# Kernel optimization log

Hardware: AMD Instinct MI355X
Metric: run time of the kernel (lower is better)

The kernel has to match this reference:

```python
import jax, jax.numpy as jnp
import numpy as np

MAX_DEPTH = 7
DEPTH_SIZES = [4 ** d for d in range(1, MAX_DEPTH + 1)]  # nodes per depth
N_NODES = sum(DEPTH_SIZES)  # 21844
N_TIMES = 48
HIDDEN = 1024
ENC_DIM = 256
B, S = 128, 32


def setup_inputs() -> dict:
    key = jax.random.key(0)
    k = jax.random.split(key, 6)
    return {
        "prefix_embedding": jax.random.normal(k[0], (B, S, HIDDEN), dtype=jnp.float32),
        "emb_matrix": jax.random.normal(k[1], (N_NODES, ENC_DIM), dtype=jnp.float32) * 0.02,
        "W_key": jax.random.normal(k[2], (HIDDEN, ENC_DIM), dtype=jnp.float32) * (1.0 / np.sqrt(ENC_DIM)),
        "b_key": jax.random.normal(k[3], (HIDDEN,), dtype=jnp.float32) * 0.01,
        "W_time": jax.random.normal(k[4], (N_TIMES, HIDDEN), dtype=jnp.float32) * (1.0 / np.sqrt(HIDDEN)),
        "b_time": jax.random.normal(k[5], (N_TIMES,), dtype=jnp.float32) * 0.01,
    }


def reference(prefix_embedding, emb_matrix, W_key, b_key, W_time, b_time):
    # keys = embedding_to_key(make_embedding_matrix(...)): [N_NODES, HIDDEN]
    keys = emb_matrix @ W_key.T + b_key
    # bmm(prefix [B,S,H], keys^T): keys identical across batch -> shared einsum
    scores = jnp.einsum("bsh,nh->bsn", prefix_embedding, keys)  # [B,S,N_NODES]
    # multitask: per-depth gather of the contiguous node block + log_softmax
    locations = []
    off = 0
    for n in DEPTH_SIZES:
        locations.append(jax.nn.log_softmax(scores[..., off:off + n], axis=-1))
        off += n
    time = jax.nn.log_softmax(prefix_embedding @ W_time.T + b_time, axis=-1)  # [B,S,N_TIMES]
    return tuple(locations) + (time,)
```

## Files before the change

### kernel.cpp

```cpp
#include <hip/hip_runtime.h>

#define NNODES 21844
#define ENC 256
#define HID 1024
#define ROWS 4096
#define NTIMES 48

typedef __attribute__((ext_vector_type(8))) short bf16x8;
typedef __attribute__((ext_vector_type(4))) float f32x4;

__device__ const int g_off[8] = {0, 4, 20, 84, 340, 1364, 5460, 21844};
__device__ const int g_l2[7]  = {2, 4, 6, 8, 10, 12, 14};

__device__ inline unsigned short f2bf(float f) {
  unsigned int u = __float_as_uint(f);
  u += 0x7FFF + ((u >> 16) & 1);
  return (unsigned short)(u >> 16);
}

__device__ inline int depth_of(int c) {
  return (c >= 4) + (c >= 20) + (c >= 84) + (c >= 340) + (c >= 1364) + (c >= 5460);
}

__global__ __launch_bounds__(256) void prep(const float* __restrict__ prefix,
                                            const float* __restrict__ emb,
                                            const float* __restrict__ Wk,
                                            const float* __restrict__ Wt,
                                            unsigned short* __restrict__ Pb16,
                                            unsigned short* __restrict__ Eb,
                                            unsigned short* __restrict__ WkT,
                                            float* __restrict__ WtT) {
  int bid = blockIdx.x, tid = threadIdx.x;
  if (bid < 4096) {
    int i = bid * 256 + tid;
    float4 v = reinterpret_cast<const float4*>(prefix)[i];
    ushort4 o; o.x = f2bf(v.x); o.y = f2bf(v.y); o.z = f2bf(v.z); o.w = f2bf(v.w);
    reinterpret_cast<ushort4*>(Pb16)[i] = o;
  } else if (bid < 9557) {
    int i = (bid - 4096) * 256 + tid;
    float4 v = reinterpret_cast<const float4*>(emb)[i];
    ushort4 o; o.x = f2bf(v.x); o.y = f2bf(v.y); o.z = f2bf(v.z); o.w = f2bf(v.w);
    reinterpret_cast<ushort4*>(Eb)[i] = o;
  } else if (bid < 10581) {
    int i = (bid - 9557) * 256 + tid;
    int e = i >> 10, h = i & 1023;
    WkT[i] = f2bf(Wk[h * ENC + e]);
  } else {
    int i = (bid - 10581) * 256 + tid;
    int k = i / NTIMES, c = i % NTIMES;
    WtT[i] = Wt[c * HID + k];
  }
}

__global__ __launch_bounds__(256) void p2_mfma(const unsigned short* __restrict__ Ab,
                                               const unsigned short* __restrict__ Bb,
                                               unsigned short* __restrict__ P2) {
  int lane = threadIdx.x & 63, w = threadIdx.x >> 6;
  int lr = lane & 15, lg = lane >> 4;
  int m0 = blockIdx.y * 64 + w * 16;
  int nb = blockIdx.x * 64;
  f32x4 acc[4];
#pragma unroll
  for (int n = 0; n < 4; ++n) acc[n] = f32x4{0.f, 0.f, 0.f, 0.f};
  const unsigned short* Ap = Ab + (long)(m0 + lr) * HID + lg * 8;
  for (int kk = 0; kk < 32; ++kk) {
    bf16x8 a = *reinterpret_cast<const bf16x8*>(Ap + kk * 32);
#pragma unroll
    for (int n = 0; n < 4; ++n) {
      bf16x8 b = *reinterpret_cast<const bf16x8*>(Bb + (long)(nb + n * 16 + lr) * HID + kk * 32 + lg * 8);
      acc[n] = __builtin_amdgcn_mfma_f32_16x16x32_bf16(a, b, acc[n], 0, 0, 0);
    }
  }
#pragma unroll
  for (int n = 0; n < 4; ++n)
#pragma unroll
    for (int j = 0; j < 4; ++j)
      P2[(m0 + lg * 4 + j) * ENC + nb + n * 16 + lr] = f2bf(acc[n][j]);
}

#define GEMM_TILE_BODY                                                                     \
  __shared__ unsigned short As[128 * 64];                                                  \
  __shared__ unsigned short Bs[128 * 64];                                                  \
  int tid = threadIdx.x;                                                                   \
  int lane = tid & 63, w = tid >> 6;                                                       \
  int lr = lane & 15, lg = lane >> 4;                                                      \
  int wr = w >> 1, wc = w & 1;                                                             \
  int m0 = blockIdx.x * 128, n0 = blockIdx.y * 128;                                        \
  int rr = tid >> 3, c8 = tid & 7;                                                         \
  f32x4 acc[4][4];                                                                         \
  _Pragma("unroll") for (int m = 0; m < 4; ++m)                                            \
    _Pragma("unroll") for (int n = 0; n < 4; ++n) acc[m][n] = f32x4{0.f, 0.f, 0.f, 0.f};   \
  for (int kt = 0; kt < 4; ++kt) {                                                         \
    if (kt) __syncthreads();                                                               \
    _Pragma("unroll") for (int r = 0; r < 4; ++r) {                                        \
      const unsigned short* ga = P2 + (long)(m0 + r * 32 + rr) * ENC + kt * 64 + c8 * 8;   \
      __builtin_amdgcn_global_load_lds(                                                    \
          (const __attribute__((address_space(1))) unsigned int*)ga,                       \
          (__attribute__((address_space(3))) unsigned int*)(As + r * 2048 + w * 512),      \
          16, 0, 0);                                                                       \
      int er = n0 + r * 32 + rr;                                                           \
      if (er > NNODES - 1) er = NNODES - 1;                                                \
      const unsigned short* gb = E + (long)er * ENC + kt * 64 + c8 * 8;                    \
      __builtin_amdgcn_global_load_lds(                                                    \
          (const __attribute__((address_space(1))) unsigned int*)gb,                       \
          (__attribute__((address_space(3))) unsigned int*)(Bs + r * 2048 + w * 512),      \
          16, 0, 0);                                                                       \
    }                                                                                      \
    __syncthreads();                                                                       \
    _Pragma("unroll") for (int kk = 0; kk < 2; ++kk) {                                     \
      bf16x8 a[4], b[4];                                                                   \
      _Pragma("unroll") for (int m = 0; m < 4; ++m)                                        \
        a[m] = *reinterpret_cast<const bf16x8*>(As + (wr * 64 + m * 16 + lr) * 64 + kk * 32 + lg * 8); \
      _Pragma("unroll") for (int n = 0; n < 4; ++n)                                        \
        b[n] = *reinterpret_cast<const bf16x8*>(Bs + (wc * 64 + n * 16 + lr) * 64 + kk * 32 + lg * 8); \
      _Pragma("unroll") for (int m = 0; m < 4; ++m)                                        \
        _Pragma("unroll") for (int n = 0; n < 4; ++n)                                      \
          acc[m][n] = __builtin_amdgcn_mfma_f32_16x16x32_bf16(a[m], b[n], acc[m][n], 0, 0, 0); \
    }                                                                                      \
  }

__global__ __launch_bounds__(256) void gemm_lse(const unsigned short* __restrict__ P2,
                                                const unsigned short* __restrict__ E,
                                                float* __restrict__ S) {
  GEMM_TILE_BODY
  int rbase = m0 + wr * 64 + lg * 4;
  int hstart = n0 + wc * 64;
  int dlo = depth_of(hstart);
  int hend = hstart + 63; if (hend > NNODES - 1) hend = NNODES - 1;
  int dhi = depth_of(hend);
  int cd[4];
#pragma unroll
  for (int n = 0; n < 4; ++n) {
    int gc = hstart + n * 16 + lr;
    cd[n] = (gc < NNODES) ? depth_of(gc) : 99;
  }
#pragma unroll
  for (int m = 0; m < 4; ++m)
#pragma unroll
    for (int n = 0; n < 4; ++n)
#pragma unroll
      for (int j = 0; j < 4; ++j) acc[m][n][j] = __expf(acc[m][n][j]);
  for (int dt = dlo; dt <= dhi; ++dt) {
#pragma unroll
    for (int m = 0; m < 4; ++m) {
      float s[4] = {0.f, 0.f, 0.f, 0.f};
#pragma unroll
      for (int n = 0; n < 4; ++n) {
        bool use = (cd[n] == dt);
#pragma unroll
        for (int j = 0; j < 4; ++j) s[j] += use ? acc[m][n][j] : 0.f;
      }
#pragma unroll
      for (int j = 0; j < 4; ++j)
#pragma unroll
        for (int o = 1; o < 16; o <<= 1) s[j] += __shfl_xor(s[j], o);
      if (lr == 0) {
#pragma unroll
        for (int j = 0; j < 4; ++j)
          atomicAdd(&S[dt * ROWS + rbase + m * 16 + j], s[j]);
      }
    }
  }
}

__global__ __launch_bounds__(256) void lse_log(const float* __restrict__ S,
                                               float* __restrict__ L) {
  int i = blockIdx.x * 256 + threadIdx.x;
  L[i] = __logf(S[i]);
}

__global__ __launch_bounds__(256) void gemm_write(const unsigned short* __restrict__ P2,
                                                  const unsigned short* __restrict__ E,
                                                  const float* __restrict__ Lse,
                                                  float* __restrict__ out) {
  GEMM_TILE_BODY
  int rbase = m0 + wr * 64 + lg * 4;
  int hstart = n0 + wc * 64;
#pragma unroll
  for (int n = 0; n < 4; ++n) {
    int gc = hstart + n * 16 + lr;
    if (gc >= NNODES) continue;
    int d = depth_of(gc);
    long ob = ((long)g_off[d] << 12) + (gc - g_off[d]);
    int sh = g_l2[d];
    const float* lp = Lse + d * ROWS;
#pragma unroll
    for (int m = 0; m < 4; ++m)
#pragma unroll
      for (int j = 0; j < 4; ++j) {
        int row = rbase + m * 16 + j;
        out[ob + ((long)row << sh)] = acc[m][n][j] - lp[row];
      }
  }
}

__global__ __launch_bounds__(256) void time_head(const float* __restrict__ prefix,
                                                 const float* __restrict__ WtT,
                                                 const float* __restrict__ bt,
                                                 float* __restrict__ out) {
  int lane = threadIdx.x & 63;
  int row = blockIdx.x * 4 + (threadIdx.x >> 6);
  const float4* pr = reinterpret_cast<const float4*>(prefix + (long)row * HID);
  float acc = -3.4e38f;
  if (lane < NTIMES) {
    float a = 0.f;
#pragma unroll 4
    for (int q = 0; q < HID / 4; ++q) {
      float4 pv = pr[q];
      const float* wrow = WtT + q * 4 * NTIMES;
      a += pv.x * wrow[lane] + pv.y * wrow[NTIMES + lane] +
           pv.z * wrow[2 * NTIMES + lane] + pv.w * wrow[3 * NTIMES + lane];
    }
    acc = a + bt[lane];
  }
  float m = acc;
#pragma unroll
  for (int d = 32; d; d >>= 1) m = fmaxf(m, __shfl_xor(m, d));
  float e = (lane < NTIMES) ? __expf(acc - m) : 0.f;
  float s = e;
#pragma unroll
  for (int d = 32; d; d >>= 1) s += __shfl_xor(s, d);
  if (lane < NTIMES) out[89473024 + row * NTIMES + lane] = acc - m - __logf(s);
}

extern "C" void kernel_launch(void* const* d_in, const int* in_sizes, int n_in,
                              void* d_out, int out_size, void* d_ws, size_t ws_size,
                              hipStream_t stream) {
  const float* prefix = (const float*)d_in[0];
  const float* emb    = (const float*)d_in[1];
  const float* Wk     = (const float*)d_in[2];
  const float* Wt     = (const float*)d_in[4];
  const float* bt     = (const float*)d_in[5];
  float* out = (float*)d_out;
  char* ws = (char*)d_ws;

  unsigned short* P2   = (unsigned short*)(ws + 0);
  unsigned short* Eb   = (unsigned short*)(ws + 2097152);
  unsigned short* WkT  = (unsigned short*)(ws + 13281280);
  unsigned short* Pb16 = (unsigned short*)(ws + 13805568);
  float*          WtT  = (float*)(ws + 22194176);
  float*          S    = (float*)(ws + 22390784);
  float*          Lse  = (float*)(ws + 22505472);

  hipMemsetAsync(S, 0, 7 * ROWS * sizeof(float), stream);

  prep<<<10773, 256, 0, stream>>>(prefix, emb, Wk, Wt, Pb16, Eb, WkT, WtT);

  p2_mfma<<<dim3(4, 64), 256, 0, stream>>>(Pb16, WkT, P2);

  gemm_lse<<<dim3(32, 171), 256, 0, stream>>>(P2, Eb, S);

  lse_log<<<112, 256, 0, stream>>>(S, Lse);

  gemm_write<<<dim3(32, 171), 256, 0, stream>>>(P2, Eb, Lse, out);

  time_head<<<1024, 256, 0, stream>>>(prefix, WtT, bt, out);
}
```

Measured before the change: 366.8 us.

## Replace second GEMM pass with stashed scores and a coalesced log-softmax subtract pass

Scores are now computed once: the GEMM kernel stores raw scores into a buffer laid out like the output while it accumulates the exp-sums. That buffer is bf16 when the workspace is large enough, and fp32 written straight into the output otherwise. A new vectorized elementwise kernel reads the stored scores, takes the log of the per-depth sums, and writes the normalized outputs with coalesced float4 stores. Zeroing of the sum buffer is folded into the prep kernel, which removes the memset and the separate log kernel. This drops a full recompute of the score GEMM at the cost of an extra round trip of the large score tensor through memory, plus bf16 rounding of scores on the stash path.

```diff
diff --git a/kernel.cpp b/kernel.cpp
--- a/kernel.cpp
+++ b/kernel.cpp
@@ -7,10 +7,10 @@
 #define NTIMES 48
 
 typedef __attribute__((ext_vector_type(8))) short bf16x8;
+typedef __attribute__((ext_vector_type(8))) unsigned short u16x8;
 typedef __attribute__((ext_vector_type(4))) float f32x4;
 
 __device__ const int g_off[8] = {0, 4, 20, 84, 340, 1364, 5460, 21844};
-__device__ const int g_l2[7]  = {2, 4, 6, 8, 10, 12, 14};
 
 __device__ inline unsigned short f2bf(float f) {
   unsigned int u = __float_as_uint(f);
@@ -29,7 +29,8 @@
                                             unsigned short* __restrict__ Pb16,
                                             unsigned short* __restrict__ Eb,
                                             unsigned short* __restrict__ WkT,
-                                            float* __restrict__ WtT) {
+                                            float* __restrict__ WtT,
+                                            float* __restrict__ S) {
   int bid = blockIdx.x, tid = threadIdx.x;
   if (bid < 4096) {
     int i = bid * 256 + tid;
@@ -45,10 +46,13 @@
     int i = (bid - 9557) * 256 + tid;
     int e = i >> 10, h = i & 1023;
     WkT[i] = f2bf(Wk[h * ENC + e]);
-  } else {
+  } else if (bid < 10773) {
     int i = (bid - 10581) * 256 + tid;
     int k = i / NTIMES, c = i % NTIMES;
     WtT[i] = Wt[c * HID + k];
+  } else {
+    int i = (bid - 10773) * 256 + tid;
+    reinterpret_cast<float4*>(S)[i] = float4{0.f, 0.f, 0.f, 0.f};
   }
 }
 
@@ -119,12 +123,33 @@
     }                                                                                      \
   }
 
-__global__ __launch_bounds__(256) void gemm_lse(const unsigned short* __restrict__ P2,
-                                                const unsigned short* __restrict__ E,
-                                                float* __restrict__ S) {
+template <int BF16S>
+__global__ __launch_bounds__(256) void gemm_stash(const unsigned short* __restrict__ P2,
+                                                  const unsigned short* __restrict__ E,
+                                                  unsigned short* __restrict__ stash,
+                                                  float* __restrict__ outp,
+                                                  float* __restrict__ S) {
   GEMM_TILE_BODY
   int rbase = m0 + wr * 64 + lg * 4;
   int hstart = n0 + wc * 64;
+#pragma unroll
+  for (int n = 0; n < 4; ++n) {
+    int gc = hstart + n * 16 + lr;
+    if (gc < NNODES) {
+      int d = depth_of(gc);
+      long ob = ((long)g_off[d] << 12) + (gc - g_off[d]);
+      int sh = 2 * (d + 1);
+#pragma unroll
+      for (int m = 0; m < 4; ++m)
+#pragma unroll
+        for (int j = 0; j < 4; ++j) {
+          int row = rbase + m * 16 + j;
+          long idx = ob + ((long)row << sh);
+          if (BF16S) stash[idx] = f2bf(acc[m][n][j]);
+          else       outp[idx]  = acc[m][n][j];
+        }
+    }
+  }
   int dlo = depth_of(hstart);
   int hend = hstart + 63; if (hend > NNODES - 1) hend = NNODES - 1;
   int dhi = depth_of(hend);
@@ -163,35 +188,42 @@
   }
 }
 
-__global__ __launch_bounds__(256) void lse_log(const float* __restrict__ S,
-                                               float* __restrict__ L) {
-  int i = blockIdx.x * 256 + threadIdx.x;
-  L[i] = __logf(S[i]);
-}
-
-__global__ __launch_bounds__(256) void gemm_write(const unsigned short* __restrict__ P2,
-                                                  const unsigned short* __restrict__ E,
-                                                  const float* __restrict__ Lse,
-                                                  float* __restrict__ out) {
-  GEMM_TILE_BODY
-  int rbase = m0 + wr * 64 + lg * 4;
-  int hstart = n0 + wc * 64;
-#pragma unroll
-  for (int n = 0; n < 4; ++n) {
-    int gc = hstart + n * 16 + lr;
-    if (gc >= NNODES) continue;
-    int d = depth_of(gc);
-    long ob = ((long)g_off[d] << 12) + (gc - g_off[d]);
-    int sh = g_l2[d];
-    const float* lp = Lse + d * ROWS;
-#pragma unroll
-    for (int m = 0; m < 4; ++m)
-#pragma unroll
-      for (int j = 0; j < 4; ++j) {
-        int row = rbase + m * 16 + j;
-        out[ob + ((long)row << sh)] = acc[m][n][j] - lp[row];
-      }
-  }
+template <int BF16S>
+__global__ __launch_bounds__(256) void sub_write(const unsigned short* __restrict__ stash,
+                                                 const float* __restrict__ S,
+                                                 float* __restrict__ out) {
+  long base = (long)blockIdx.x * 2048 + threadIdx.x * 8;
+  int d = (base >= 16384) + (base >= 81920) + (base >= 344064) +
+          (base >= 1392640) + (base >= 5586944) + (base >= 22364160);
+  long bd = (d == 0) ? 0L : (d == 1) ? 16384L : (d == 2) ? 81920L : (d == 3) ? 344064L
+          : (d == 4) ? 1392640L : (d == 5) ? 5586944L : 22364160L;
+  long rel = base - bd;
+  const float* sp = S + d * ROWS;
+  float v[8];
+  if (BF16S) {
+    u16x8 u = *reinterpret_cast<const u16x8*>(stash + base);
+#pragma unroll
+    for (int j = 0; j < 8; ++j) v[j] = __uint_as_float((unsigned)(unsigned short)u[j] << 16);
+  } else {
+    float4 a = reinterpret_cast<const float4*>(out + base)[0];
+    float4 b = reinterpret_cast<const float4*>(out + base)[1];
+    v[0] = a.x; v[1] = a.y; v[2] = a.z; v[3] = a.w;
+    v[4] = b.x; v[5] = b.y; v[6] = b.z; v[7] = b.w;
+  }
+  float4 o0, o1;
+  if (d == 0) {
+    int r0 = (int)(rel >> 2);
+    float l0 = __logf(sp[r0]), l1 = __logf(sp[r0 + 1]);
+    o0 = float4{v[0] - l0, v[1] - l0, v[2] - l0, v[3] - l0};
+    o1 = float4{v[4] - l1, v[5] - l1, v[6] - l1, v[7] - l1};
+  } else {
+    int row = (int)(rel >> (2 * (d + 1)));
+    float l = __logf(sp[row]);
+    o0 = float4{v[0] - l, v[1] - l, v[2] - l, v[3] - l};
+    o1 = float4{v[4] - l, v[5] - l, v[6] - l, v[7] - l};
+  }
+  reinterpret_cast<float4*>(out + base)[0] = o0;
+  reinterpret_cast<float4*>(out + base)[1] = o1;
 }
 
 __global__ __launch_bounds__(256) void time_head(const float* __restrict__ prefix,
@@ -234,25 +266,28 @@
   float* out = (float*)d_out;
   char* ws = (char*)d_ws;
 
-  unsigned short* P2   = (unsigned short*)(ws + 0);
-  unsigned short* Eb   = (unsigned short*)(ws + 2097152);
-  unsigned short* WkT  = (unsigned short*)(ws + 13281280);
-  unsigned short* Pb16 = (unsigned short*)(ws + 13805568);
-  float*          WtT  = (float*)(ws + 22194176);
-  float*          S    = (float*)(ws + 22390784);
-  float*          Lse  = (float*)(ws + 22505472);
-
-  hipMemsetAsync(S, 0, 7 * ROWS * sizeof(float), stream);
-
-  prep<<<10773, 256, 0, stream>>>(prefix, emb, Wk, Wt, Pb16, Eb, WkT, WtT);
+  unsigned short* P2    = (unsigned short*)(ws + 0);
+  unsigned short* Eb    = (unsigned short*)(ws + 2097152);
+  unsigned short* WkT   = (unsigned short*)(ws + 13281280);
+  unsigned short* Pb16  = (unsigned short*)(ws + 13805568);
+  float*          WtT   = (float*)(ws + 22194176);
+  float*          S     = (float*)(ws + 22390784);
+  unsigned short* stash = (unsigned short*)(ws + 22505472);
+  const size_t WS_NEED_STASH = 22505472UL + 178946048UL;
+
+  bool big = ws_size >= WS_NEED_STASH;
+
+  prep<<<10801, 256, 0, stream>>>(prefix, emb, Wk, Wt, Pb16, Eb, WkT, WtT, S);
 
   p2_mfma<<<dim3(4, 64), 256, 0, stream>>>(Pb16, WkT, P2);
 
-  gemm_lse<<<dim3(32, 171), 256, 0, stream>>>(P2, Eb, S);
-
-  lse_log<<<112, 256, 0, stream>>>(S, Lse);
-
-  gemm_write<<<dim3(32, 171), 256, 0, stream>>>(P2, Eb, Lse, out);
+  if (big) {
+    gemm_stash<1><<<dim3(32, 171), 256, 0, stream>>>(P2, Eb, stash, out, S);
+    sub_write<1><<<43688, 256, 0, stream>>>(stash, S, out);
+  } else {
+    gemm_stash<0><<<dim3(32, 171), 256, 0, stream>>>(P2, Eb, stash, out, S);
+    sub_write<0><<<43688, 256, 0, stream>>>(stash, S, out);
+  }
 
   time_head<<<1024, 256, 0, stream>>>(prefix, WtT, bt, out);
 }
```

New measurement: 345.7 us. 1.06x faster.
